# Performance work log

Measured on AMD Instinct MI355X. Metric: run time of the kernel, lower is better.

The kernel has to match this reference:

```python
import jax, jax.numpy as jnp
import numpy as np

INV_SQRT_2 = 0.7071067811865476


def setup_inputs() -> dict:
    key = jax.random.key(0)
    k1, k2, k3, k4, k5 = jax.random.split(key, 5)
    batch, nodes, edges, dim_in, dim_out = 2, 10000, 320000, 64, 64
    x = jax.random.normal(k1, (batch, nodes, dim_in, 3), dtype=jnp.float32)
    src = jax.random.randint(k2, (edges,), 0, nodes, dtype=jnp.int32)
    dst = jax.random.randint(k3, (edges,), 0, nodes, dtype=jnp.int32)
    # VecLinear weights (no bias; equivariant linear over the channel dim)
    W_src = jax.random.normal(k4, (dim_out, dim_in), dtype=jnp.float32) / np.sqrt(dim_in)
    W_dst = jax.random.normal(k5, (dim_out, dim_in), dtype=jnp.float32) / np.sqrt(dim_in)
    return {"x": x, "W_src": W_src, "W_dst": W_dst, "src": src, "dst": dst}


def reference(x, W_src, W_dst, src, dst):
    # x: (b, nodes, dim_in, 3); gather node feats per edge, mix channels, combine.
    xs = jnp.take(x, src, axis=1)  # (b, edges, dim_in, 3)
    xd = jnp.take(x, dst, axis=1)  # (b, edges, dim_in, 3)
    ys = jnp.einsum('oi,beiv->beov', W_src, xs)
    yd = jnp.einsum('oi,beiv->beov', W_dst, xd)
    return (ys + yd) * INV_SQRT_2  # (b, edges, dim_out, 3)
```

## Files before the change

### kernel.cpp

```cpp
#include <hip/hip_runtime.h>

#define INV_SQRT_2F 0.70710678118654752440f

typedef float fvec4 __attribute__((ext_vector_type(4)));

static __device__ __forceinline__ unsigned short f2bf(float f)
{
    unsigned int u = __float_as_uint(f);
    u += 0x7fffu + ((u >> 16) & 1u);
    return (unsigned short)(u >> 16);
}

__global__ void __launch_bounds__(128)
node_transform(const float* __restrict__ x,
               const float* __restrict__ W_src,
               const float* __restrict__ W_dst,
               unsigned short* __restrict__ y_src,
               unsigned short* __restrict__ y_dst,
               int nodes, int bn_total)
{
    __shared__ float xs[192];
    int bn = blockIdx.x;
    if (bn >= bn_total) return;
    int b = bn / nodes;
    int n = bn - b * nodes;

    const float4* xp = (const float4*)(x + (size_t)bn * 192);
    int t = threadIdx.x;
    if (t < 48) ((float4*)xs)[t] = xp[t];
    __syncthreads();

    int o = t & 63;
    const float*    W = (t < 64) ? W_src : W_dst;
    unsigned short* y = (t < 64) ? y_src : y_dst;

    const float4* Wrow = (const float4*)(W + o * 64);
    float a0 = 0.f, a1 = 0.f, a2 = 0.f;
#pragma unroll
    for (int i4 = 0; i4 < 16; ++i4) {
        float4 w = Wrow[i4];
        int i = i4 * 4;
        a0 = fmaf(w.x, xs[(i + 0) * 3 + 0], a0);
        a1 = fmaf(w.x, xs[(i + 0) * 3 + 1], a1);
        a2 = fmaf(w.x, xs[(i + 0) * 3 + 2], a2);
        a0 = fmaf(w.y, xs[(i + 1) * 3 + 0], a0);
        a1 = fmaf(w.y, xs[(i + 1) * 3 + 1], a1);
        a2 = fmaf(w.y, xs[(i + 1) * 3 + 2], a2);
        a0 = fmaf(w.z, xs[(i + 2) * 3 + 0], a0);
        a1 = fmaf(w.z, xs[(i + 2) * 3 + 1], a1);
        a2 = fmaf(w.z, xs[(i + 2) * 3 + 2], a2);
        a0 = fmaf(w.w, xs[(i + 3) * 3 + 0], a0);
        a1 = fmaf(w.w, xs[(i + 3) * 3 + 1], a1);
        a2 = fmaf(w.w, xs[(i + 3) * 3 + 2], a2);
    }
    unsigned short* yp = y + ((size_t)n * 2 + b) * 192 + o * 3;
    yp[0] = f2bf(a0);
    yp[1] = f2bf(a1);
    yp[2] = f2bf(a2);
}

__global__ void __launch_bounds__(256)
edge_combine(const unsigned short* __restrict__ y_src,
             const unsigned short* __restrict__ y_dst,
             const int* __restrict__ src,
             const int* __restrict__ dst,
             float* __restrict__ out,
             int edges)
{
    const int total  = edges * 48;
    const int stride = gridDim.x * blockDim.x;
    const uint2* ys = (const uint2*)y_src;
    const uint2* yd = (const uint2*)y_dst;
    fvec4*       o4 = (fvec4*)out;

    for (int t = blockIdx.x * blockDim.x + threadIdx.x; t < total; t += stride) {
        int e = t / 48;
        int j = t - e * 48;
        size_t sb = (size_t)src[e] * 96 + j;
        size_t db = (size_t)dst[e] * 96 + j;

        uint2 a0 = ys[sb];
        uint2 b0 = yd[db];
        uint2 a1 = ys[sb + 48];
        uint2 b1 = yd[db + 48];

        fvec4 r0, r1;
        r0.x = (__uint_as_float(a0.x << 16)          + __uint_as_float(b0.x << 16))          * INV_SQRT_2F;
        r0.y = (__uint_as_float(a0.x & 0xffff0000u)  + __uint_as_float(b0.x & 0xffff0000u))  * INV_SQRT_2F;
        r0.z = (__uint_as_float(a0.y << 16)          + __uint_as_float(b0.y << 16))          * INV_SQRT_2F;
        r0.w = (__uint_as_float(a0.y & 0xffff0000u)  + __uint_as_float(b0.y & 0xffff0000u))  * INV_SQRT_2F;
        r1.x = (__uint_as_float(a1.x << 16)          + __uint_as_float(b1.x << 16))          * INV_SQRT_2F;
        r1.y = (__uint_as_float(a1.x & 0xffff0000u)  + __uint_as_float(b1.x & 0xffff0000u))  * INV_SQRT_2F;
        r1.z = (__uint_as_float(a1.y << 16)          + __uint_as_float(b1.y << 16))          * INV_SQRT_2F;
        r1.w = (__uint_as_float(a1.y & 0xffff0000u)  + __uint_as_float(b1.y & 0xffff0000u))  * INV_SQRT_2F;

        __builtin_nontemporal_store(r0, &o4[(size_t)e * 48 + j]);
        __builtin_nontemporal_store(r1, &o4[((size_t)edges + e) * 48 + j]);
    }
}

__global__ void __launch_bounds__(64)
edge_fused(const float* __restrict__ x,
           const float* __restrict__ W_src,
           const float* __restrict__ W_dst,
           const int* __restrict__ src,
           const int* __restrict__ dst,
           float* __restrict__ out,
           int edges, int nodes)
{
    __shared__ float xs[192];
    __shared__ float xd[192];
    int be = blockIdx.x;
    int b  = be / edges;
    int e  = be - b * edges;
    int s  = src[e];
    int d  = dst[e];
    const float* xps = x + ((size_t)b * nodes + s) * 192;
    const float* xpd = x + ((size_t)b * nodes + d) * 192;
    int t = threadIdx.x;
#pragma unroll
    for (int k = 0; k < 3; ++k) {
        xs[t + 64 * k] = xps[t + 64 * k];
        xd[t + 64 * k] = xpd[t + 64 * k];
    }
    __syncthreads();
    float a0 = 0.f, a1 = 0.f, a2 = 0.f;
#pragma unroll
    for (int i = 0; i < 64; ++i) {
        float ws = W_src[t * 64 + i];
        float wd = W_dst[t * 64 + i];
        a0 += ws * xs[i * 3 + 0] + wd * xd[i * 3 + 0];
        a1 += ws * xs[i * 3 + 1] + wd * xd[i * 3 + 1];
        a2 += ws * xs[i * 3 + 2] + wd * xd[i * 3 + 2];
    }
    float* op = out + ((size_t)b * edges + e) * 192 + t * 3;
    op[0] = a0 * INV_SQRT_2F;
    op[1] = a1 * INV_SQRT_2F;
    op[2] = a2 * INV_SQRT_2F;
}

extern "C" void kernel_launch(void* const* d_in, const int* in_sizes, int n_in,
                              void* d_out, int out_size, void* d_ws, size_t ws_size,
                              hipStream_t stream)
{
    const float* x     = (const float*)d_in[0];
    const float* W_src = (const float*)d_in[1];
    const float* W_dst = (const float*)d_in[2];
    const int*   src   = (const int*)d_in[3];
    const int*   dst   = (const int*)d_in[4];
    float*       out   = (float*)d_out;

    const int batch = 2;
    const int edges = in_sizes[3];
    const int nodes = in_sizes[0] / (batch * 192);

    const size_t y_elems = (size_t)batch * nodes * 192;
    const size_t needed  = 2 * y_elems * sizeof(unsigned short);

    if (ws_size >= needed) {
        unsigned short* y_src = (unsigned short*)d_ws;
        unsigned short* y_dst = y_src + y_elems;
        const int bn_total = batch * nodes;
        node_transform<<<bn_total, 128, 0, stream>>>(x, W_src, W_dst,
                                                     y_src, y_dst, nodes, bn_total);
        edge_combine<<<2048, 256, 0, stream>>>(y_src, y_dst, src, dst, out, edges);
    } else {
        edge_fused<<<batch * edges, 64, 0, stream>>>(x, W_src, W_dst,
                                                     src, dst, out, edges, nodes);
    }
}
```

Before: 216.5 us.

## Bucket edges by source node before gather-combine for gather locality

Adds a counting sort of edges by source node (histogram, single-block scan, atomic scatter) into a packed (src,dst,edge id) array. The combine kernel then walks edges in source order, so consecutive edges reuse the same y_src rows in cache, and writes each output row back to its original edge slot. In exchange it adds four extra kernel launches, atomic traffic and a serial single-block scan. The output writes also become scattered rather than sequential.

After: 241.0 us. 11.3% more time.

```diff
diff --git a/kernel.cpp b/kernel.cpp
--- a/kernel.cpp
+++ b/kernel.cpp
@@ -9,6 +9,62 @@
     unsigned int u = __float_as_uint(f);
     u += 0x7fffu + ((u >> 16) & 1u);
     return (unsigned short)(u >> 16);
+}
+
+__global__ void zero_u32(unsigned int* __restrict__ p, int n)
+{
+    int i = blockIdx.x * blockDim.x + threadIdx.x;
+    if (i < n) p[i] = 0u;
+}
+
+__global__ void hist_src(const int* __restrict__ src,
+                         unsigned int* __restrict__ cnt, int edges)
+{
+    int i = blockIdx.x * blockDim.x + threadIdx.x;
+    int stride = gridDim.x * blockDim.x;
+    for (; i < edges; i += stride) atomicAdd(&cnt[src[i]], 1u);
+}
+
+__global__ void __launch_bounds__(1024)
+scan_offsets(const unsigned int* __restrict__ cnt,
+             unsigned int* __restrict__ cursor, int n)
+{
+    __shared__ unsigned int part[1024];
+    int t = threadIdx.x;
+    int per = (n + 1023) / 1024;
+    int lo = t * per;
+    int hi = lo + per; if (hi > n) hi = n;
+    unsigned int s = 0;
+    for (int i = lo; i < hi; ++i) s += cnt[i];
+    part[t] = s;
+    __syncthreads();
+    for (int d = 1; d < 1024; d <<= 1) {
+        unsigned int v = (t >= d) ? part[t - d] : 0u;
+        __syncthreads();
+        part[t] += v;
+        __syncthreads();
+    }
+    unsigned int base = (t > 0) ? part[t - 1] : 0u;
+    for (int i = lo; i < hi; ++i) {
+        unsigned int c = cnt[i];
+        cursor[i] = base;
+        base += c;
+    }
+}
+
+__global__ void scatter_edges(const int* __restrict__ src,
+                              const int* __restrict__ dst,
+                              unsigned int* __restrict__ cursor,
+                              uint2* __restrict__ sde, int edges)
+{
+    int i = blockIdx.x * blockDim.x + threadIdx.x;
+    int stride = gridDim.x * blockDim.x;
+    for (; i < edges; i += stride) {
+        unsigned int s = (unsigned int)src[i];
+        unsigned int d = (unsigned int)dst[i];
+        unsigned int pos = atomicAdd(&cursor[s], 1u);
+        sde[pos] = make_uint2((s << 16) | d, (unsigned int)i);
+    }
 }
 
 __global__ void __launch_bounds__(128)
@@ -60,6 +116,50 @@
 }
 
 __global__ void __launch_bounds__(256)
+edge_combine_sorted(const unsigned short* __restrict__ y_src,
+                    const unsigned short* __restrict__ y_dst,
+                    const uint2* __restrict__ sde,
+                    float* __restrict__ out,
+                    int edges)
+{
+    const int total  = edges * 48;
+    const int stride = gridDim.x * blockDim.x;
+    const uint2* ys = (const uint2*)y_src;
+    const uint2* yd = (const uint2*)y_dst;
+    fvec4*       o4 = (fvec4*)out;
+
+    for (int t = blockIdx.x * blockDim.x + threadIdx.x; t < total; t += stride) {
+        int pe = t / 48;
+        int j  = t - pe * 48;
+        uint2 se = sde[pe];
+        unsigned int s = se.x >> 16;
+        unsigned int d = se.x & 0xffffu;
+        unsigned int e = se.y;
+
+        size_t sb = (size_t)s * 96 + j;
+        size_t db = (size_t)d * 96 + j;
+
+        uint2 a0 = ys[sb];
+        uint2 b0 = yd[db];
+        uint2 a1 = ys[sb + 48];
+        uint2 b1 = yd[db + 48];
+
+        fvec4 r0, r1;
+        r0.x = (__uint_as_float(a0.x << 16)         + __uint_as_float(b0.x << 16))         * INV_SQRT_2F;
+        r0.y = (__uint_as_float(a0.x & 0xffff0000u) + __uint_as_float(b0.x & 0xffff0000u)) * INV_SQRT_2F;
+        r0.z = (__uint_as_float(a0.y << 16)         + __uint_as_float(b0.y << 16))         * INV_SQRT_2F;
+        r0.w = (__uint_as_float(a0.y & 0xffff0000u) + __uint_as_float(b0.y & 0xffff0000u)) * INV_SQRT_2F;
+        r1.x = (__uint_as_float(a1.x << 16)         + __uint_as_float(b1.x << 16))         * INV_SQRT_2F;
+        r1.y = (__uint_as_float(a1.x & 0xffff0000u) + __uint_as_float(b1.x & 0xffff0000u)) * INV_SQRT_2F;
+        r1.z = (__uint_as_float(a1.y << 16)         + __uint_as_float(b1.y << 16))         * INV_SQRT_2F;
+        r1.w = (__uint_as_float(a1.y & 0xffff0000u) + __uint_as_float(b1.y & 0xffff0000u)) * INV_SQRT_2F;
+
+        __builtin_nontemporal_store(r0, &o4[(size_t)e * 48 + j]);
+        __builtin_nontemporal_store(r1, &o4[((size_t)edges + e) * 48 + j]);
+    }
+}
+
+__global__ void __launch_bounds__(256)
 edge_combine(const unsigned short* __restrict__ y_src,
              const unsigned short* __restrict__ y_dst,
              const int* __restrict__ src,
@@ -85,14 +185,14 @@
         uint2 b1 = yd[db + 48];
 
         fvec4 r0, r1;
-        r0.x = (__uint_as_float(a0.x << 16)          + __uint_as_float(b0.x << 16))          * INV_SQRT_2F;
-        r0.y = (__uint_as_float(a0.x & 0xffff0000u)  + __uint_as_float(b0.x & 0xffff0000u))  * INV_SQRT_2F;
-        r0.z = (__uint_as_float(a0.y << 16)          + __uint_as_float(b0.y << 16))          * INV_SQRT_2F;
-        r0.w = (__uint_as_float(a0.y & 0xffff0000u)  + __uint_as_float(b0.y & 0xffff0000u))  * INV_SQRT_2F;
-        r1.x = (__uint_as_float(a1.x << 16)          + __uint_as_float(b1.x << 16))          * INV_SQRT_2F;
-        r1.y = (__uint_as_float(a1.x & 0xffff0000u)  + __uint_as_float(b1.x & 0xffff0000u))  * INV_SQRT_2F;
-        r1.z = (__uint_as_float(a1.y << 16)          + __uint_as_float(b1.y << 16))          * INV_SQRT_2F;
-        r1.w = (__uint_as_float(a1.y & 0xffff0000u)  + __uint_as_float(b1.y & 0xffff0000u))  * INV_SQRT_2F;
+        r0.x = (__uint_as_float(a0.x << 16)         + __uint_as_float(b0.x << 16))         * INV_SQRT_2F;
+        r0.y = (__uint_as_float(a0.x & 0xffff0000u) + __uint_as_float(b0.x & 0xffff0000u)) * INV_SQRT_2F;
+        r0.z = (__uint_as_float(a0.y << 16)         + __uint_as_float(b0.y << 16))         * INV_SQRT_2F;
+        r0.w = (__uint_as_float(a0.y & 0xffff0000u) + __uint_as_float(b0.y & 0xffff0000u)) * INV_SQRT_2F;
+        r1.x = (__uint_as_float(a1.x << 16)         + __uint_as_float(b1.x << 16))         * INV_SQRT_2F;
+        r1.y = (__uint_as_float(a1.x & 0xffff0000u) + __uint_as_float(b1.x & 0xffff0000u)) * INV_SQRT_2F;
+        r1.z = (__uint_as_float(a1.y << 16)         + __uint_as_float(b1.y << 16))         * INV_SQRT_2F;
+        r1.w = (__uint_as_float(a1.y & 0xffff0000u) + __uint_as_float(b1.y & 0xffff0000u)) * INV_SQRT_2F;
 
         __builtin_nontemporal_store(r0, &o4[(size_t)e * 48 + j]);
         __builtin_nontemporal_store(r1, &o4[((size_t)edges + e) * 48 + j]);
@@ -155,11 +255,33 @@
     const int nodes = in_sizes[0] / (batch * 192);
 
     const size_t y_elems = (size_t)batch * nodes * 192;
-    const size_t needed  = 2 * y_elems * sizeof(unsigned short);
-
-    if (ws_size >= needed) {
-        unsigned short* y_src = (unsigned short*)d_ws;
-        unsigned short* y_dst = y_src + y_elems;
+    const size_t y_bytes = ((y_elems * 2 + 255) / 256) * 256;
+    const size_t cnt_bytes = (((size_t)nodes * 4 + 255) / 256) * 256;
+    const size_t sde_bytes = ((size_t)edges * 8 + 255) / 256 * 256;
+    const size_t needed_sorted = 2 * y_bytes + 2 * cnt_bytes + sde_bytes;
+    const size_t needed_plain  = 2 * y_bytes;
+
+    char* wsb = (char*)d_ws;
+
+    if (ws_size >= needed_sorted && nodes <= 65535) {
+        unsigned short* y_src  = (unsigned short*)wsb;
+        unsigned short* y_dst  = (unsigned short*)(wsb + y_bytes);
+        unsigned int*   cnt    = (unsigned int*)(wsb + 2 * y_bytes);
+        unsigned int*   cursor = (unsigned int*)(wsb + 2 * y_bytes + cnt_bytes);
+        uint2*          sde    = (uint2*)(wsb + 2 * y_bytes + 2 * cnt_bytes);
+
+        const int bn_total = batch * nodes;
+        node_transform<<<bn_total, 128, 0, stream>>>(x, W_src, W_dst,
+                                                     y_src, y_dst, nodes, bn_total);
+        zero_u32<<<(nodes + 255) / 256, 256, 0, stream>>>(cnt, nodes);
+        int egrid = (edges + 255) / 256; if (egrid > 2048) egrid = 2048;
+        hist_src<<<egrid, 256, 0, stream>>>(src, cnt, edges);
+        scan_offsets<<<1, 1024, 0, stream>>>(cnt, cursor, nodes);
+        scatter_edges<<<egrid, 256, 0, stream>>>(src, dst, cursor, sde, edges);
+        edge_combine_sorted<<<2048, 256, 0, stream>>>(y_src, y_dst, sde, out, edges);
+    } else if (ws_size >= needed_plain) {
+        unsigned short* y_src = (unsigned short*)wsb;
+        unsigned short* y_dst = (unsigned short*)(wsb + y_bytes);
         const int bn_total = batch * nodes;
         node_transform<<<bn_total, 128, 0, stream>>>(x, W_src, W_dst,
                                                      y_src, y_dst, nodes, bn_total);
```
